# Optimization experiments

Hardware: AMD Instinct MI355X
Metric: run time of the kernel (lower is better)

The kernel has to match this reference:

```python
import jax, jax.numpy as jnp
import numpy as np

IN_DIM, HID, OUT_DIM, PRED_LEN = 33, 64, 2, 25
B, P, T = 1024, 22, 20
EPS = 1e-5


def _lstm_step(Wih, Whh, b, h, c, xt):
    # PyTorch gate order: i, f, g, o
    gates = xt @ Wih.T + h @ Whh.T + b
    i, f, g, o = jnp.split(gates, 4, axis=-1)
    c_new = jax.nn.sigmoid(f) * c + jax.nn.sigmoid(i) * jnp.tanh(g)
    h_new = jax.nn.sigmoid(o) * jnp.tanh(c_new)
    return h_new, c_new


def setup_inputs() -> dict:
    key = jax.random.key(0)
    ks = jax.random.split(key, 20)
    s = 0.1
    inp = {
        "x": jax.random.normal(ks[0], (B, P, T, IN_DIM), dtype=jnp.float32),
        "enc_Wih": jax.random.normal(ks[1], (4 * HID, IN_DIM)) * s,
        "enc_Whh": jax.random.normal(ks[2], (4 * HID, HID)) * s,
        "enc_bih": jax.random.normal(ks[3], (4 * HID,)) * s,
        "enc_bhh": jax.random.normal(ks[4], (4 * HID,)) * s,
        "q_W": jax.random.normal(ks[5], (HID, HID)) * s,
        "q_b": jax.random.normal(ks[6], (HID,)) * s,
        "k_W": jax.random.normal(ks[7], (HID, HID)) * s,
        "k_b": jax.random.normal(ks[8], (HID,)) * s,
        "v_W": jax.random.normal(ks[9], (HID, HID)) * s,
        "v_b": jax.random.normal(ks[10], (HID,)) * s,
        "ln_g": jnp.ones((HID,), jnp.float32),
        "ln_b": jnp.zeros((HID,), jnp.float32),
        "dec_Wih": jax.random.normal(ks[11], (4 * HID, OUT_DIM)) * s,
        "dec_Whh": jax.random.normal(ks[12], (4 * HID, HID)) * s,
        "dec_bih": jax.random.normal(ks[13], (4 * HID,)) * s,
        "dec_bhh": jax.random.normal(ks[14], (4 * HID,)) * s,
        "fc_W": jax.random.normal(ks[15], (OUT_DIM, HID)) * s,
        "fc_b": jax.random.normal(ks[16], (OUT_DIM,)) * s,
    }
    return inp


def reference(x, enc_Wih, enc_Whh, enc_bih, enc_bhh, q_W, q_b, k_W, k_b,
              v_W, v_b, ln_g, ln_b, dec_Wih, dec_Whh, dec_bih, dec_bhh,
              fc_W, fc_b):
    b, p, t, d = x.shape
    n = b * p
    xf = x.reshape(n, t, d)

    # ----- encoder LSTM over history -----
    b_enc = enc_bih + enc_bhh
    def enc_step(carry, xt):
        h, c = carry
        h, c = _lstm_step(enc_Wih, enc_Whh, b_enc, h, c, xt)
        return (h, c), None
    h0 = jnp.zeros((n, HID), x.dtype)
    (hn, cn), _ = jax.lax.scan(enc_step, (h0, h0), xf.transpose(1, 0, 2))

    # ----- interaction GNN (self-attention over players) -----
    last_hidden = hn.reshape(b, p, HID)
    Q = last_hidden @ q_W.T + q_b
    K = last_hidden @ k_W.T + k_b
    V = last_hidden @ v_W.T + v_b
    scores = jnp.einsum('bph,bqh->bpq', Q, K) / jnp.sqrt(jnp.float32(HID))
    attn = jax.nn.softmax(scores, axis=-1)
    ctx = jnp.einsum('bpq,bqh->bph', attn, V)

    # ----- layernorm(residual) -----
    y = last_hidden + ctx
    mu = y.mean(-1, keepdims=True)
    var = y.var(-1, keepdims=True)
    y = (y - mu) / jnp.sqrt(var + EPS) * ln_g + ln_b

    b_dec = dec_bih + dec_bhh
    def dec_step(carry, _):
        h, c, inp = carry
        h, c = _lstm_step(dec_Wih, dec_Whh, b_dec, h, c, inp)
        pred = h @ fc_W.T + fc_b
        return (h, c, pred), pred
    inp0 = xf[:, -1, :OUT_DIM]
    _, preds = jax.lax.scan(dec_step, (y.reshape(n, HID), cn, inp0),
                            None, length=PRED_LEN)  # [PRED_LEN, n, 2]
    return preds.transpose(1, 0, 2).reshape(b, p, PRED_LEN, OUT_DIM)
```

## Files before the change

### kernel.cpp

```cpp
#include <hip/hip_runtime.h>

typedef short short8 __attribute__((ext_vector_type(8)));
typedef float f32x4 __attribute__((ext_vector_type(4)));

#define IN_DIM   33
#define HID      64
#define OUT_DIM  2
#define PRED_LEN 25
#define NB       1024
#define NP       22
#define NT       20
#define EPS      1e-5f

#define SWZ(s,k) (((s) << 7) + ((k) ^ (((s) & 7) << 3)))

__device__ __forceinline__ float fast_rcp(float x){ return __builtin_amdgcn_rcpf(x); }
__device__ __forceinline__ float sigm(float x){ return fast_rcp(1.0f + __expf(-x)); }
__device__ __forceinline__ float tanhf_(float x){ float e = __expf(2.0f*x); return 1.0f - 2.0f*fast_rcp(e + 1.0f); }
__device__ __forceinline__ unsigned short bf_hi(float f){
    unsigned u = __float_as_uint(f);
    return (unsigned short)((u + 0x7fffu + ((u >> 16) & 1u)) >> 16);
}
__device__ __forceinline__ float bf_f(unsigned short h){ return __uint_as_float(((unsigned)h) << 16); }

__global__ __launch_bounds__(256, 2) void nfl_mfma(
    const float* __restrict__ x,
    const float* __restrict__ enc_Wih, const float* __restrict__ enc_Whh,
    const float* __restrict__ enc_bih, const float* __restrict__ enc_bhh,
    const float* __restrict__ q_W, const float* __restrict__ q_b,
    const float* __restrict__ k_W, const float* __restrict__ k_b,
    const float* __restrict__ v_W, const float* __restrict__ v_b,
    const float* __restrict__ ln_g, const float* __restrict__ ln_b,
    const float* __restrict__ dec_Wih, const float* __restrict__ dec_Whh,
    const float* __restrict__ dec_bih, const float* __restrict__ dec_bhh,
    const float* __restrict__ fc_W, const float* __restrict__ fc_b,
    float* __restrict__ out)
{
    __shared__ unsigned short shA_hi[32*128];
    __shared__ unsigned short shA_lo[32*128];
    __shared__ float sh_f[32*66];
    __shared__ float sh_q[32*66];
    __shared__ float sh_k[32*66];
    __shared__ float sh_v[32*66];
    __shared__ float sh_sc[22*24];
    __shared__ float sh_p0[32];
    __shared__ float sh_p1[32];
    __shared__ float sh_mu[22];
    __shared__ float sh_rs[22];

    const int tid  = threadIdx.x;
    const int w    = tid >> 6;
    const int ln   = tid & 63;
    const int lo15 = ln & 15;
    const int qq   = ln >> 4;
    const int jh   = 16*w + lo15;
    const int b    = blockIdx.x;
    const float* xb = x + (size_t)b * NP*NT*IN_DIM;

    for (int i = tid; i < 32*128; i += 256){ shA_hi[i] = 0; shA_lo[i] = 0; }

    short8 eBh[4][4], eBl[4][4];
    float bias_e[4];
    #pragma unroll
    for (int nt = 0; nt < 4; nt++){
        int g = 16*w + 64*nt + lo15;
        bias_e[nt] = enc_bih[g] + enc_bhh[g];
        #pragma unroll
        for (int kt = 0; kt < 4; kt++){
            #pragma unroll
            for (int e = 0; e < 8; e++){
                int k = 32*kt + 8*qq + e;
                float v;
                if (k < HID) v = enc_Whh[g*HID + k];
                else { int d = k - HID; v = (d < IN_DIM) ? enc_Wih[g*IN_DIM + d] : 0.0f; }
                unsigned short h = bf_hi(v); float hf = bf_f(h);
                eBh[nt][kt][e] = (short)h;
                eBl[nt][kt][e] = (short)bf_hi(v - hf);
            }
        }
    }

    float cst[2][4] = {{0,0,0,0},{0,0,0,0}};
    __syncthreads();

    for (int t = 0; t < NT; t++){
        for (int i = tid; i < NP*IN_DIM; i += 256){
            int s = i / IN_DIM, d = i - s*IN_DIM;
            float v = xb[(s*NT + t)*IN_DIM + d];
            unsigned short h = bf_hi(v); float hf = bf_f(h);
            int idx = SWZ(s, HID + d);
            shA_hi[idx] = h; shA_lo[idx] = bf_hi(v - hf);
        }
        __syncthreads();

        f32x4 acc[2][4];
        #pragma unroll
        for (int m = 0; m < 2; m++)
            #pragma unroll
            for (int nt = 0; nt < 4; nt++){
                float bb = bias_e[nt];
                acc[m][nt][0]=bb; acc[m][nt][1]=bb; acc[m][nt][2]=bb; acc[m][nt][3]=bb;
            }
        #pragma unroll
        for (int kt = 0; kt < 4; kt++){
            #pragma unroll
            for (int m = 0; m < 2; m++){
                int idx = SWZ(16*m + lo15, 32*kt + 8*qq);
                short8 ah = *reinterpret_cast<const short8*>(&shA_hi[idx]);
                short8 al = *reinterpret_cast<const short8*>(&shA_lo[idx]);
                #pragma unroll
                for (int nt = 0; nt < 4; nt++){
                    acc[m][nt] = __builtin_amdgcn_mfma_f32_16x16x32_bf16(ah, eBh[nt][kt], acc[m][nt], 0,0,0);
                    acc[m][nt] = __builtin_amdgcn_mfma_f32_16x16x32_bf16(al, eBh[nt][kt], acc[m][nt], 0,0,0);
                    acc[m][nt] = __builtin_amdgcn_mfma_f32_16x16x32_bf16(ah, eBl[nt][kt], acc[m][nt], 0,0,0);
                }
            }
        }
        __syncthreads();

        #pragma unroll
        for (int m = 0; m < 2; m++){
            #pragma unroll
            for (int j = 0; j < 4; j++){
                float gi = acc[m][0][j], gf = acc[m][1][j], gg = acc[m][2][j], go = acc[m][3][j];
                float c = sigm(gf)*cst[m][j] + sigm(gi)*tanhf_(gg);
                cst[m][j] = c;
                float h = sigm(go)*tanhf_(c);
                int s = 16*m + 4*qq + j;
                unsigned short hh = bf_hi(h); float hf2 = bf_f(hh);
                int idx = SWZ(s, jh);
                shA_hi[idx] = hh; shA_lo[idx] = bf_hi(h - hf2);
                if (t == NT-1) sh_f[s*66 + jh] = h;
            }
        }
        __syncthreads();
    }

    {
        short8 qBh[3][2], qBl[3][2];
        float qb3[3];
        #pragma unroll
        for (int mat = 0; mat < 3; mat++){
            const float* W  = (mat==0) ? q_W : (mat==1) ? k_W : v_W;
            const float* bb = (mat==0) ? q_b : (mat==1) ? k_b : v_b;
            qb3[mat] = bb[jh];
            #pragma unroll
            for (int kt = 0; kt < 2; kt++){
                #pragma unroll
                for (int e = 0; e < 8; e++){
                    int k = 32*kt + 8*qq + e;
                    float v = W[jh*HID + k];
                    unsigned short h = bf_hi(v); float hf = bf_f(h);
                    qBh[mat][kt][e] = (short)h;
                    qBl[mat][kt][e] = (short)bf_hi(v - hf);
                }
            }
        }
        f32x4 qacc[3][2];
        #pragma unroll
        for (int mat = 0; mat < 3; mat++)
            #pragma unroll
            for (int m = 0; m < 2; m++){
                float bb = qb3[mat];
                qacc[mat][m][0]=bb; qacc[mat][m][1]=bb; qacc[mat][m][2]=bb; qacc[mat][m][3]=bb;
            }
        #pragma unroll
        for (int kt = 0; kt < 2; kt++){
            #pragma unroll
            for (int m = 0; m < 2; m++){
                int idx = SWZ(16*m + lo15, 32*kt + 8*qq);
                short8 ah = *reinterpret_cast<const short8*>(&shA_hi[idx]);
                short8 al = *reinterpret_cast<const short8*>(&shA_lo[idx]);
                #pragma unroll
                for (int mat = 0; mat < 3; mat++){
                    qacc[mat][m] = __builtin_amdgcn_mfma_f32_16x16x32_bf16(ah, qBh[mat][kt], qacc[mat][m], 0,0,0);
                    qacc[mat][m] = __builtin_amdgcn_mfma_f32_16x16x32_bf16(al, qBh[mat][kt], qacc[mat][m], 0,0,0);
                    qacc[mat][m] = __builtin_amdgcn_mfma_f32_16x16x32_bf16(ah, qBl[mat][kt], qacc[mat][m], 0,0,0);
                }
            }
        }
        #pragma unroll
        for (int mat = 0; mat < 3; mat++){
            float* dst = (mat==0) ? sh_q : (mat==1) ? sh_k : sh_v;
            #pragma unroll
            for (int m = 0; m < 2; m++)
                #pragma unroll
                for (int j = 0; j < 4; j++)
                    dst[(16*m + 4*qq + j)*66 + jh] = qacc[mat][m][j];
        }
    }
    __syncthreads();

    for (int i = tid; i < NP*NP; i += 256){
        int p = i / NP, q = i - p*NP;
        float acc = 0.0f;
        #pragma unroll
        for (int k = 0; k < HID; k++) acc = fmaf(sh_q[p*66 + k], sh_k[q*66 + k], acc);
        sh_sc[p*24 + q] = acc * 0.125f;
    }
    __syncthreads();

    if (tid < NP){
        float m = -1e30f;
        for (int q = 0; q < NP; q++) m = fmaxf(m, sh_sc[tid*24 + q]);
        float sum = 0.0f;
        for (int q = 0; q < NP; q++){ float e = __expf(sh_sc[tid*24 + q] - m); sh_sc[tid*24 + q] = e; sum += e; }
        float inv = fast_rcp(sum);
        for (int q = 0; q < NP; q++) sh_sc[tid*24 + q] *= inv;
    }
    __syncthreads();

    for (int i = tid; i < NP*HID; i += 256){
        int s = i >> 6, j = i & 63;
        float acc = 0.0f;
        #pragma unroll
        for (int q = 0; q < NP; q++) acc = fmaf(sh_sc[s*24 + q], sh_v[q*66 + j], acc);
        sh_f[s*66 + j] += acc;
    }
    __syncthreads();

    if (tid < NP){
        float mu = 0.0f;
        for (int j = 0; j < HID; j++) mu += sh_f[tid*66 + j];
        mu *= (1.0f/HID);
        float var = 0.0f;
        for (int j = 0; j < HID; j++){ float d = sh_f[tid*66 + j] - mu; var += d*d; }
        sh_mu[tid] = mu;
        sh_rs[tid] = rsqrtf(var*(1.0f/HID) + EPS);
    }
    __syncthreads();

    for (int i = tid; i < NP*HID; i += 256){
        int s = i >> 6, j = i & 63;
        float v = (sh_f[s*66 + j] - sh_mu[s]) * sh_rs[s] * ln_g[j] + ln_b[j];
        unsigned short h = bf_hi(v); float hf = bf_f(h);
        int idx = SWZ(s, j);
        shA_hi[idx] = h; shA_lo[idx] = bf_hi(v - hf);
    }
    if (tid < 32){
        float v0 = 0.0f, v1 = 0.0f;
        if (tid < NP){
            v0 = xb[(tid*NT + NT-1)*IN_DIM + 0];
            v1 = xb[(tid*NT + NT-1)*IN_DIM + 1];
        }
        sh_p0[tid] = v0; sh_p1[tid] = v1;
    }

    short8 dBh[4][2], dBl[4][2];
    float bias_d[4], wd0[4], wd1[4];
    #pragma unroll
    for (int nt = 0; nt < 4; nt++){
        int g = 16*w + 64*nt + lo15;
        bias_d[nt] = dec_bih[g] + dec_bhh[g];
        wd0[nt] = dec_Wih[g*OUT_DIM + 0];
        wd1[nt] = dec_Wih[g*OUT_DIM + 1];
        #pragma unroll
        for (int kt = 0; kt < 2; kt++){
            #pragma unroll
            for (int e = 0; e < 8; e++){
                int k = 32*kt + 8*qq + e;
                float v = dec_Whh[g*HID + k];
                unsigned short h = bf_hi(v); float hf = bf_f(h);
                dBh[nt][kt][e] = (short)h;
                dBl[nt][kt][e] = (short)bf_hi(v - hf);
            }
        }
    }
    const int fitem = tid >> 2, fq = tid & 3, fs = fitem >> 1, fo = fitem & 1;
    float fcw[16]; float fcb = 0.0f;
    if (tid < 176){
        #pragma unroll
        for (int jj = 0; jj < 16; jj++) fcw[jj] = fc_W[fo*HID + 16*fq + jj];
        fcb = fc_b[fo];
    }
    float* outb = out + (size_t)b * NP * PRED_LEN * OUT_DIM;
    __syncthreads();

    for (int t = 0; t < PRED_LEN; t++){
        f32x4 acc[2][4];
        #pragma unroll
        for (int m = 0; m < 2; m++){
            #pragma unroll
            for (int j = 0; j < 4; j++){
                int s = 16*m + 4*qq + j;
                float p0 = sh_p0[s], p1 = sh_p1[s];
                #pragma unroll
                for (int nt = 0; nt < 4; nt++)
                    acc[m][nt][j] = bias_d[nt] + wd0[nt]*p0 + wd1[nt]*p1;
            }
        }
        #pragma unroll
        for (int kt = 0; kt < 2; kt++){
            #pragma unroll
            for (int m = 0; m < 2; m++){
                int idx = SWZ(16*m + lo15, 32*kt + 8*qq);
                short8 ah = *reinterpret_cast<const short8*>(&shA_hi[idx]);
                short8 al = *reinterpret_cast<const short8*>(&shA_lo[idx]);
                #pragma unroll
                for (int nt = 0; nt < 4; nt++){
                    acc[m][nt] = __builtin_amdgcn_mfma_f32_16x16x32_bf16(ah, dBh[nt][kt], acc[m][nt], 0,0,0);
                    acc[m][nt] = __builtin_amdgcn_mfma_f32_16x16x32_bf16(al, dBh[nt][kt], acc[m][nt], 0,0,0);
                    acc[m][nt] = __builtin_amdgcn_mfma_f32_16x16x32_bf16(ah, dBl[nt][kt], acc[m][nt], 0,0,0);
                }
            }
        }
        __syncthreads();

        #pragma unroll
        for (int m = 0; m < 2; m++){
            #pragma unroll
            for (int j = 0; j < 4; j++){
                float gi = acc[m][0][j], gf = acc[m][1][j], gg = acc[m][2][j], go = acc[m][3][j];
                float c = sigm(gf)*cst[m][j] + sigm(gi)*tanhf_(gg);
                cst[m][j] = c;
                float h = sigm(go)*tanhf_(c);
                int s = 16*m + 4*qq + j;
                unsigned short hh = bf_hi(h); float hf2 = bf_f(hh);
                int idx = SWZ(s, jh);
                shA_hi[idx] = hh; shA_lo[idx] = bf_hi(h - hf2);
            }
        }
        __syncthreads();

        if (tid < 176){
            int idx0 = SWZ(fs, 16*fq);
            int idx1 = SWZ(fs, 16*fq + 8);
            short8 h0h = *reinterpret_cast<const short8*>(&shA_hi[idx0]);
            short8 h0l = *reinterpret_cast<const short8*>(&shA_lo[idx0]);
            short8 h1h = *reinterpret_cast<const short8*>(&shA_hi[idx1]);
            short8 h1l = *reinterpret_cast<const short8*>(&shA_lo[idx1]);
            float part = 0.0f;
            #pragma unroll
            for (int e = 0; e < 8; e++){
                part = fmaf(bf_f((unsigned short)h0h[e]) + bf_f((unsigned short)h0l[e]), fcw[e],     part);
                part = fmaf(bf_f((unsigned short)h1h[e]) + bf_f((unsigned short)h1l[e]), fcw[8 + e], part);
            }
            part += __shfl_xor(part, 1);
            part += __shfl_xor(part, 2);
            if (fq == 0){
                float pred = part + fcb;
                outb[(fs*PRED_LEN + t)*OUT_DIM + fo] = pred;
                if (fo == 0) sh_p0[fs] = pred; else sh_p1[fs] = pred;
            }
        }
        __syncthreads();
    }
}

extern "C" void kernel_launch(void* const* d_in, const int* in_sizes, int n_in,
                              void* d_out, int out_size, void* d_ws, size_t ws_size,
                              hipStream_t stream) {
    const float* x        = (const float*)d_in[0];
    const float* enc_Wih  = (const float*)d_in[1];
    const float* enc_Whh  = (const float*)d_in[2];
    const float* enc_bih  = (const float*)d_in[3];
    const float* enc_bhh  = (const float*)d_in[4];
    const float* q_W      = (const float*)d_in[5];
    const float* q_b      = (const float*)d_in[6];
    const float* k_W      = (const float*)d_in[7];
    const float* k_b      = (const float*)d_in[8];
    const float* v_W      = (const float*)d_in[9];
    const float* v_b      = (const float*)d_in[10];
    const float* ln_g     = (const float*)d_in[11];
    const float* ln_b     = (const float*)d_in[12];
    const float* dec_Wih  = (const float*)d_in[13];
    const float* dec_Whh  = (const float*)d_in[14];
    const float* dec_bih  = (const float*)d_in[15];
    const float* dec_bhh  = (const float*)d_in[16];
    const float* fc_W     = (const float*)d_in[17];
    const float* fc_b     = (const float*)d_in[18];
    float* out = (float*)d_out;

    nfl_mfma<<<dim3(NB), dim3(256), 0, stream>>>(
        x, enc_Wih, enc_Whh, enc_bih, enc_bhh,
        q_W, q_b, k_W, k_b, v_W, v_b, ln_g, ln_b,
        dec_Wih, dec_Whh, dec_bih, dec_bhh, fc_W, fc_b, out);
}
```

Before: 388.3 us.

## Alias LDS buffers, raise occupancy, overlap x staging, pack bf16 conversions

Shrinks shared memory by aliasing the K/V buffers onto the hi/lo staging arena and sizing per-player arrays to 22 rows. It raises the launch-bounds occupancy hint from 2 to 4 blocks per CU. Loading of the next timestep's x is moved into the nonlinearity phase, which removes one barrier per encoder step. The hi/lo bf16 split now uses the packed v_cvt_pk_bf16_f32 instruction. The higher occupancy target may force register spills, since each thread holds many short8 weight fragments.

```diff
diff --git a/kernel.cpp b/kernel.cpp
--- a/kernel.cpp
+++ b/kernel.cpp
@@ -22,8 +22,13 @@
     return (unsigned short)((u + 0x7fffu + ((u >> 16) & 1u)) >> 16);
 }
 __device__ __forceinline__ float bf_f(unsigned short h){ return __uint_as_float(((unsigned)h) << 16); }
-
-__global__ __launch_bounds__(256, 2) void nfl_mfma(
+__device__ __forceinline__ unsigned cvt_pk_bf16(float a, float b){
+    unsigned r;
+    asm("v_cvt_pk_bf16_f32 %0, %1, %2" : "=v"(r) : "v"(a), "v"(b));
+    return r;
+}
+
+__global__ __launch_bounds__(256, 4) void nfl_mfma(
     const float* __restrict__ x,
     const float* __restrict__ enc_Wih, const float* __restrict__ enc_Whh,
     const float* __restrict__ enc_bih, const float* __restrict__ enc_bhh,
@@ -36,17 +41,19 @@
     const float* __restrict__ fc_W, const float* __restrict__ fc_b,
     float* __restrict__ out)
 {
-    __shared__ unsigned short shA_hi[32*128];
-    __shared__ unsigned short shA_lo[32*128];
-    __shared__ float sh_f[32*66];
-    __shared__ float sh_q[32*66];
-    __shared__ float sh_k[32*66];
-    __shared__ float sh_v[32*66];
-    __shared__ float sh_sc[22*24];
+    __shared__ __align__(16) unsigned char arena[32*128*2*2];
+    __shared__ float sh_q [NP*66];
+    __shared__ float sh_f [NP*66];
+    __shared__ float sh_sc[NP*24];
     __shared__ float sh_p0[32];
     __shared__ float sh_p1[32];
-    __shared__ float sh_mu[22];
-    __shared__ float sh_rs[22];
+    __shared__ float sh_mu[NP];
+    __shared__ float sh_rs[NP];
+
+    unsigned short* shA_hi = (unsigned short*)arena;
+    unsigned short* shA_lo = (unsigned short*)(arena + 8192);
+    float* sh_k = (float*)arena;
+    float* sh_v = (float*)(arena + 8192);
 
     const int tid  = threadIdx.x;
     const int w    = tid >> 6;
@@ -57,8 +64,6 @@
     const int b    = blockIdx.x;
     const float* xb = x + (size_t)b * NP*NT*IN_DIM;
 
-    for (int i = tid; i < 32*128; i += 256){ shA_hi[i] = 0; shA_lo[i] = 0; }
-
     short8 eBh[4][4], eBl[4][4];
     float bias_e[4];
     #pragma unroll
@@ -73,26 +78,71 @@
                 float v;
                 if (k < HID) v = enc_Whh[g*HID + k];
                 else { int d = k - HID; v = (d < IN_DIM) ? enc_Wih[g*IN_DIM + d] : 0.0f; }
-                unsigned short h = bf_hi(v); float hf = bf_f(h);
+                unsigned short h = bf_hi(v);
                 eBh[nt][kt][e] = (short)h;
-                eBl[nt][kt][e] = (short)bf_hi(v - hf);
-            }
-        }
-    }
+                eBl[nt][kt][e] = (short)bf_hi(v - bf_f(h));
+            }
+        }
+    }
+
+    for (int i = tid; i < 32*128; i += 256) ((unsigned*)arena)[i] = 0;
 
     float cst[2][4] = {{0,0,0,0},{0,0,0,0}};
     __syncthreads();
 
+    auto stage_x = [&](int t){
+        for (int i = tid; i < NP*IN_DIM; i += 256){
+            int s = i / IN_DIM, d = i - s * IN_DIM;
+            float v = xb[(s*NT + t)*IN_DIM + d];
+            unsigned short h = bf_hi(v);
+            int idx = SWZ(s, HID + d);
+            shA_hi[idx] = h; shA_lo[idx] = bf_hi(v - bf_f(h));
+        }
+    };
+
+    auto nonlin_store = [&](f32x4 (&acc)[2][4], bool save_f){
+        #pragma unroll
+        for (int m = 0; m < 2; m++){
+            #pragma unroll
+            for (int jp = 0; jp < 2; jp++){
+                const int j0 = 2*jp;
+                float hh0, hh1;
+                {
+                    float gi=acc[m][0][j0], gf=acc[m][1][j0], gg=acc[m][2][j0], go=acc[m][3][j0];
+                    float c = sigm(gf)*cst[m][j0] + sigm(gi)*tanhf_(gg);
+                    cst[m][j0] = c;
+                    hh0 = sigm(go)*tanhf_(c);
+                }
+                {
+                    float gi=acc[m][0][j0+1], gf=acc[m][1][j0+1], gg=acc[m][2][j0+1], go=acc[m][3][j0+1];
+                    float c = sigm(gf)*cst[m][j0+1] + sigm(gi)*tanhf_(gg);
+                    cst[m][j0+1] = c;
+                    hh1 = sigm(go)*tanhf_(c);
+                }
+                unsigned hp = cvt_pk_bf16(hh0, hh1);
+                float r0 = hh0 - __uint_as_float(hp << 16);
+                float r1 = hh1 - __uint_as_float(hp & 0xffff0000u);
+                unsigned lp = cvt_pk_bf16(r0, r1);
+                const int s0 = 16*m + 4*qq + j0;
+                if (s0 < NP){
+                    int i0 = SWZ(s0, jh);
+                    shA_hi[i0] = (unsigned short)hp;
+                    shA_lo[i0] = (unsigned short)lp;
+                    if (save_f) sh_f[s0*66 + jh] = hh0;
+                }
+                if (s0 + 1 < NP){
+                    int i1 = SWZ(s0 + 1, jh);
+                    shA_hi[i1] = (unsigned short)(hp >> 16);
+                    shA_lo[i1] = (unsigned short)(lp >> 16);
+                    if (save_f) sh_f[(s0+1)*66 + jh] = hh1;
+                }
+            }
+        }
+    };
+
+    stage_x(0);
+    __syncthreads();
     for (int t = 0; t < NT; t++){
-        for (int i = tid; i < NP*IN_DIM; i += 256){
-            int s = i / IN_DIM, d = i - s*IN_DIM;
-            float v = xb[(s*NT + t)*IN_DIM + d];
-            unsigned short h = bf_hi(v); float hf = bf_f(h);
-            int idx = SWZ(s, HID + d);
-            shA_hi[idx] = h; shA_lo[idx] = bf_hi(v - hf);
-        }
-        __syncthreads();
-
         f32x4 acc[2][4];
         #pragma unroll
         for (int m = 0; m < 2; m++)
@@ -117,22 +167,8 @@
             }
         }
         __syncthreads();
-
-        #pragma unroll
-        for (int m = 0; m < 2; m++){
-            #pragma unroll
-            for (int j = 0; j < 4; j++){
-                float gi = acc[m][0][j], gf = acc[m][1][j], gg = acc[m][2][j], go = acc[m][3][j];
-                float c = sigm(gf)*cst[m][j] + sigm(gi)*tanhf_(gg);
-                cst[m][j] = c;
-                float h = sigm(go)*tanhf_(c);
-                int s = 16*m + 4*qq + j;
-                unsigned short hh = bf_hi(h); float hf2 = bf_f(hh);
-                int idx = SWZ(s, jh);
-                shA_hi[idx] = hh; shA_lo[idx] = bf_hi(h - hf2);
-                if (t == NT-1) sh_f[s*66 + jh] = h;
-            }
-        }
+        if (t + 1 < NT) stage_x(t + 1);
+        nonlin_store(acc, t == NT-1);
         __syncthreads();
     }
 
@@ -150,9 +186,9 @@
                 for (int e = 0; e < 8; e++){
                     int k = 32*kt + 8*qq + e;
                     float v = W[jh*HID + k];
-                    unsigned short h = bf_hi(v); float hf = bf_f(h);
+                    unsigned short h = bf_hi(v);
                     qBh[mat][kt][e] = (short)h;
-                    qBl[mat][kt][e] = (short)bf_hi(v - hf);
+                    qBl[mat][kt][e] = (short)bf_hi(v - bf_f(h));
                 }
             }
         }
@@ -179,14 +215,17 @@
                 }
             }
         }
+        __syncthreads();
         #pragma unroll
         for (int mat = 0; mat < 3; mat++){
             float* dst = (mat==0) ? sh_q : (mat==1) ? sh_k : sh_v;
             #pragma unroll
             for (int m = 0; m < 2; m++)
                 #pragma unroll
-                for (int j = 0; j < 4; j++)
-                    dst[(16*m + 4*qq + j)*66 + jh] = qacc[mat][m][j];
+                for (int j = 0; j < 4; j++){
+                    int s = 16*m + 4*qq + j;
+                    if (s < NP) dst[s*66 + jh] = qacc[mat][m][j];
+                }
         }
     }
     __syncthreads();
@@ -230,12 +269,18 @@
     }
     __syncthreads();
 
-    for (int i = tid; i < NP*HID; i += 256){
-        int s = i >> 6, j = i & 63;
-        float v = (sh_f[s*66 + j] - sh_mu[s]) * sh_rs[s] * ln_g[j] + ln_b[j];
-        unsigned short h = bf_hi(v); float hf = bf_f(h);
-        int idx = SWZ(s, j);
-        shA_hi[idx] = h; shA_lo[idx] = bf_hi(v - hf);
+    for (int i = tid; i < NP*HID/2; i += 256){
+        int s = i >> 5, j0 = (i & 31) << 1;
+        float sc = sh_rs[s], mu = sh_mu[s];
+        float v0 = (sh_f[s*66 + j0]   - mu) * sc * ln_g[j0]   + ln_b[j0];
+        float v1 = (sh_f[s*66 + j0+1] - mu) * sc * ln_g[j0+1] + ln_b[j0+1];
+        unsigned hp = cvt_pk_bf16(v0, v1);
+        float r0 = v0 - __uint_as_float(hp << 16);
+        float r1 = v1 - __uint_as_float(hp & 0xffff0000u);
+        unsigned lp = cvt_pk_bf16(r0, r1);
+        int idx = SWZ(s, j0);
+        *(unsigned*)&shA_hi[idx] = hp;
+        *(unsigned*)&shA_lo[idx] = lp;
     }
     if (tid < 32){
         float v0 = 0.0f, v1 = 0.0f;
@@ -260,9 +305,9 @@
             for (int e = 0; e < 8; e++){
                 int k = 32*kt + 8*qq + e;
                 float v = dec_Whh[g*HID + k];
-                unsigned short h = bf_hi(v); float hf = bf_f(h);
+                unsigned short h = bf_hi(v);
                 dBh[nt][kt][e] = (short)h;
-                dBl[nt][kt][e] = (short)bf_hi(v - hf);
+                dBl[nt][kt][e] = (short)bf_hi(v - bf_f(h));
             }
         }
     }
@@ -306,20 +351,7 @@
         }
         __syncthreads();
 
-        #pragma unroll
-        for (int m = 0; m < 2; m++){
-            #pragma unroll
-            for (int j = 0; j < 4; j++){
-                float gi = acc[m][0][j], gf = acc[m][1][j], gg = acc[m][2][j], go = acc[m][3][j];
-                float c = sigm(gf)*cst[m][j] + sigm(gi)*tanhf_(gg);
-                cst[m][j] = c;
-                float h = sigm(go)*tanhf_(c);
-                int s = 16*m + 4*qq + j;
-                unsigned short hh = bf_hi(h); float hf2 = bf_f(hh);
-                int idx = SWZ(s, jh);
-                shA_hi[idx] = hh; shA_lo[idx] = bf_hi(h - hf2);
-            }
-        }
+        nonlin_store(acc, false);
         __syncthreads();
 
         if (tid < 176){
```

Result: slower. 977.9 us (+151.8%).
